# Performance work log

Measured on AMD Instinct MI355X. Metric: run time of the kernel, lower is better.

## Reference

```python
import jax, jax.numpy as jnp
import numpy as np

B, C, H, W = 8, 256, 48, 48
CK = 64  # C // k
WSCALE = 0.3 / np.sqrt(C)  # keep exp(QK^T) finite (original has no 1/sqrt(d) scaling)


def conv1x1(x, w, b):
    # x: (B,C,H,W), w: (O,C,1,1), b: (O,) -> (B,O,H,W)
    return jnp.einsum('bchw,oc->bohw', x, w[:, :, 0, 0]) + b[None, :, None, None]


def setup_inputs() -> dict:
    key = jax.random.key(0)
    ks = jax.random.split(key, 6)
    x = jax.random.normal(ks[0], (B, C, H, W), dtype=jnp.float32)
    qw = jax.random.normal(ks[1], (CK, C, 1, 1), dtype=jnp.float32) * WSCALE
    kw = jax.random.normal(ks[2], (CK, C, 1, 1), dtype=jnp.float32) * WSCALE
    vw = jax.random.normal(ks[3], (C, C, 1, 1), dtype=jnp.float32) * (1.0 / np.sqrt(C))
    gw = jax.random.normal(ks[4], (C, C, 1, 1), dtype=jnp.float32) * (1.0 / np.sqrt(C))
    zk = jnp.zeros((CK,), dtype=jnp.float32)
    zc = jnp.zeros((C,), dtype=jnp.float32)
    return {
        'x': x,
        'query_weight': qw, 'query_bias': zk,
        'key_weight': kw, 'key_bias': zk,
        'value_weight': vw, 'value_bias': zc,
        'gamma_weight': gw, 'gamma_bias': zc,
        'k': 4,
    }


def reference(x, query_weight, query_bias, key_weight, key_bias,
              value_weight, value_bias, gamma_weight, gamma_bias, k):
    b, c, h, w = x.shape
    n = h * w
    q = conv1x1(x, query_weight, query_bias).reshape(b, -1, n)   # (B,Ck,N)
    kk = conv1x1(x, key_weight, key_bias).reshape(b, -1, n)      # (B,Ck,N)
    # energy[b,i,j] = q_i . k_j  (queries on rows, no sqrt(d) scaling)
    energy = jnp.einsum('bci,bcj->bij', q, kk)                   # (B,N,N)
    energy = jnp.exp(energy)
    energy = energy / jnp.sum(energy, axis=2, keepdims=True)     # unnormalized-softmax over keys
    v = conv1x1(x, value_weight, value_bias).reshape(b, c, n)    # (B,C,N)
    # out[b,c,j] = sum_i v[b,c,i] * energy[b,i,j]  (faithful to torch.bmm(V, energy))
    out = jnp.einsum('bci,bij->bcj', v, energy).reshape(b, c, h, w)
    out = conv1x1(out, gamma_weight, gamma_bias)
    return out
```

## Files before the change

kernel.cpp:

```cpp
#include <hip/hip_runtime.h>

#define BATCH 8
#define CIN   256
#define NPIX  2304
#define CKD   64
#define NIT   (NPIX / 16)
#define NIC   (NPIX / 32)
#define NJB   (NPIX / 64)

typedef _Float16 f16;
typedef __attribute__((ext_vector_type(4))) _Float16 f16x4;
typedef __attribute__((ext_vector_type(8))) _Float16 f16x8;
typedef __attribute__((ext_vector_type(4))) float    f32x4;


__global__ __launch_bounds__(256) void cast_w(
    const float* __restrict__ qw, const float* __restrict__ kw,
    f16* __restrict__ Wqk)
{
    int idx = (blockIdx.x * 256 + threadIdx.x) * 4;
    const float* src = (idx < 16384) ? qw + idx : kw + (idx - 16384);
    float4 v = *(const float4*)src;
    f16x4 h = { (f16)v.x, (f16)v.y, (f16)v.z, (f16)v.w };
    *(f16x4*)&Wqk[idx] = h;
}

__global__ __launch_bounds__(256) void make_wgv(
    const float* __restrict__ gw, const float* __restrict__ vw,
    const float* __restrict__ vb,
    f16* __restrict__ Wgv, float* __restrict__ b2)
{
    const int o = blockIdx.x, c2 = threadIdx.x;
    float s = 0.f;
    for (int c = 0; c < CIN; ++c)
        s += gw[o * CIN + c] * vw[(size_t)c * CIN + c2];
    Wgv[(size_t)o * CIN + c2] = (f16)s;
    if (c2 == 0) {
        float sb = 0.f;
        for (int c = 0; c < CIN; ++c) sb += gw[o * CIN + c] * vb[c];
        b2[o] = sb;
    }
}

__global__ __launch_bounds__(256) void cast_xT(
    const float* __restrict__ x, f16* __restrict__ xT)
{
    __shared__ float s[64][65];
    const int t = threadIdx.x;
    const int n0 = blockIdx.x * 64, c0 = blockIdx.y * 64, b = blockIdx.z;
    const float* xb = x + ((size_t)b * CIN + c0) * NPIX + n0;

    const int cl = t >> 4, ng = (t & 15) * 4;
    #pragma unroll
    for (int p = 0; p < 4; ++p) {
        float4 v = *(const float4*)(xb + (size_t)(cl + 16 * p) * NPIX + ng);
        s[cl + 16 * p][ng + 0] = v.x;
        s[cl + 16 * p][ng + 1] = v.y;
        s[cl + 16 * p][ng + 2] = v.z;
        s[cl + 16 * p][ng + 3] = v.w;
    }
    __syncthreads();
    const int nl = t >> 2, cs = (t & 3) * 16;
    f16 h[16];
    #pragma unroll
    for (int j = 0; j < 16; ++j) h[j] = (f16)s[cs + j][nl];
    f16* gp = &xT[((size_t)b * NPIX + n0 + nl) * CIN + c0 + cs];
    *(f16x8*)gp       = *(f16x8*)&h[0];
    *(f16x8*)(gp + 8) = *(f16x8*)&h[8];
}

__global__ __launch_bounds__(256) void qk_conv_mfma(
    const f16* __restrict__ xT, const f16* __restrict__ Wqk,
    const float* __restrict__ qbias, const float* __restrict__ kbias,
    f16* __restrict__ q_blk, f16* __restrict__ k_blk)
{
    __shared__ __align__(16) f16 us[32 * 136];
    const int t = threadIdx.x, w = t >> 6, lane = t & 63;
    const int quad = lane >> 4, l16 = lane & 15;
    const int wm = w & 1, wn = w >> 1;
    const int n0 = blockIdx.x * 32, b = blockIdx.y;

    const f16* bp = xT + ((size_t)b * NPIX + n0 + 16 * wn + l16) * CIN;
    const f16* ap = Wqk + (size_t)(64 * wm + l16) * CIN;

    f32x4 acc[4];
    #pragma unroll
    for (int mt = 0; mt < 4; ++mt) acc[mt] = (f32x4){0.f, 0.f, 0.f, 0.f};

    #pragma unroll
    for (int kk = 0; kk < CIN; kk += 32) {
        f16x8 bf = *(const f16x8*)(bp + kk + quad * 8);
        #pragma unroll
        for (int mt = 0; mt < 4; ++mt) {
            f16x8 af = *(const f16x8*)(ap + (size_t)mt * 16 * CIN + kk + quad * 8);
            acc[mt] = __builtin_amdgcn_mfma_f32_16x16x32_f16(af, bf, acc[mt], 0, 0, 0);
        }
    }
    const float* bias = wm ? kbias - 64 : qbias;
    #pragma unroll
    for (int mt = 0; mt < 4; ++mt) {
        int ob = 64 * wm + 16 * mt + quad * 4;
        #pragma unroll
        for (int r = 0; r < 4; ++r)
            us[(16 * wn + l16) * 136 + ob + r] = (f16)(acc[mt][r] + bias[ob + r]);
    }
    __syncthreads();
    {
        int ks2 = t >> 7, nt = (t >> 6) & 1, ln = t & 63;
        const f16* usr = &us[(nt * 16 + (ln & 15)) * 136 + ks2 * 32 + (ln >> 4) * 8];
        size_t base = (((size_t)b * NIT + (n0 >> 4) + nt) * 2 + ks2) * 512 + ln * 8;
        *(f16x8*)&q_blk[base] = *(const f16x8*)(usr);
        *(f16x8*)&k_blk[base] = *(const f16x8*)(usr + 64);
    }
}

#define ESL 136
__global__ __launch_bounds__(256) void energy_S(
    const f16* __restrict__ q_blk, const f16* __restrict__ k_blk,
    float* __restrict__ Pred)
{
    __shared__ __align__(16) f16 es[64 * ESL];
    __shared__ float red2[2][128];
    const int t    = threadIdx.x;
    const int w    = t >> 6, lane = t & 63;
    const int quad = lane >> 4, l16 = lane & 15;
    const int j0 = blockIdx.x * 64, i0 = blockIdx.y * 128, b = blockIdx.z;
    const size_t ln8 = (size_t)lane * 8;
    const f16* qb = q_blk + (size_t)b * NIT * 2 * 512 + ln8;

    f32x4 acc[8];
    #pragma unroll
    for (int mt = 0; mt < 8; ++mt) acc[mt] = (f32x4){0.f, 0.f, 0.f, 0.f};

    #pragma unroll
    for (int ks = 0; ks < 2; ++ks) {
        f16x8 bf = *(const f16x8*)(k_blk +
            (((size_t)b * NIT + (j0 >> 4) + w) * 2 + ks) * 512 + ln8);
        #pragma unroll
        for (int mt = 0; mt < 8; ++mt) {
            f16x8 af = *(const f16x8*)(qb + ((size_t)((i0 >> 4) + mt) * 2 + ks) * 512);
            acc[mt] = __builtin_amdgcn_mfma_f32_16x16x32_f16(af, bf, acc[mt], 0, 0, 0);
        }
    }

    #pragma unroll
    for (int mt = 0; mt < 8; ++mt) {
        f16x4 h = { (f16)__expf(acc[mt][0]), (f16)__expf(acc[mt][1]),
                    (f16)__expf(acc[mt][2]), (f16)__expf(acc[mt][3]) };
        *(f16x4*)&es[(16 * w + l16) * ESL + 16 * mt + quad * 4] = h;
    }
    __syncthreads();
    {
        int i = t & 127, jq = t >> 7;
        float s = 0.f;
        #pragma unroll
        for (int jj = 0; jj < 32; ++jj)
            s += (float)es[(jq * 32 + jj) * ESL + i];
        red2[jq][i] = s;
    }
    __syncthreads();
    if (t < 128)
        Pred[((size_t)blockIdx.x * BATCH + b) * NPIX + i0 + t] =
            red2[0][t] + red2[1][t];
}

__global__ __launch_bounds__(256) void reduce_S(
    const float* __restrict__ Pred, float* __restrict__ S)
{
    const size_t BN = (size_t)BATCH * NPIX;
    size_t idx = (size_t)blockIdx.x * 256 + threadIdx.x;
    float s = 0.f;
    #pragma unroll
    for (int jb = 0; jb < NJB; ++jb)
        s += Pred[(size_t)jb * BN + idx];
    S[idx] = s;
}

__global__ __launch_bounds__(256) void v_conv_mfma(
    const f16* __restrict__ xT, const f16* __restrict__ Wv,
    const float* __restrict__ vbias, const float* __restrict__ S,
    f16* __restrict__ u_blk)
{
    __shared__ __align__(16) f16 smem[9216];
    f16* As = smem;
    f16* Bs = smem + 128 * 40;
    f16* us = smem;
    const int t = threadIdx.x, w = t >> 6, lane = t & 63;
    const int quad = lane >> 4, l16 = lane & 15;
    const int wm = w & 1, wn = w >> 1;
    const int i0 = blockIdx.x * 64, c0 = blockIdx.y * 128, b = blockIdx.z;
    const int sub = t >> 2, le = t & 3;
    const f16* srcA = Wv + (size_t)(c0 + sub) * CIN + le * 8;
    const f16* srcB = xT + ((size_t)b * NPIX + i0 + sub) * CIN + le * 8;
    const int ldsw = sub * 40 + le * 8;

    f32x4 acc[4][2];
    #pragma unroll
    for (int mt = 0; mt < 4; ++mt)
        #pragma unroll
        for (int nt = 0; nt < 2; ++nt)
            acc[mt][nt] = (f32x4){0.f, 0.f, 0.f, 0.f};

    for (int kk = 0; kk < CIN; kk += 32) {
        f16x8 ta0 = *(const f16x8*)(srcA + kk);
        f16x8 ta1 = *(const f16x8*)(srcA + (size_t)64 * CIN + kk);
        f16x8 tb0 = *(const f16x8*)(srcB + kk);
        __syncthreads();
        *(f16x8*)&As[ldsw]           = ta0;
        *(f16x8*)&As[64 * 40 + ldsw] = ta1;
        *(f16x8*)&Bs[ldsw]           = tb0;
        __syncthreads();
        f16x8 af[4], bf[2];
        #pragma unroll
        for (int mt = 0; mt < 4; ++mt)
            af[mt] = *(const f16x8*)&As[(64 * wm + 16 * mt + l16) * 40 + quad * 8];
        #pragma unroll
        for (int nt = 0; nt < 2; ++nt)
            bf[nt] = *(const f16x8*)&Bs[(32 * wn + 16 * nt + l16) * 40 + quad * 8];
        #pragma unroll
        for (int mt = 0; mt < 4; ++mt)
            #pragma unroll
            for (int nt = 0; nt < 2; ++nt)
                acc[mt][nt] = __builtin_amdgcn_mfma_f32_16x16x32_f16(
                    af[mt], bf[nt], acc[mt][nt], 0, 0, 0);
    }

    __syncthreads();
    #pragma unroll
    for (int nt = 0; nt < 2; ++nt) {
        int i = 32 * wn + 16 * nt + l16;
        float is = 1.0f / S[(size_t)b * NPIX + i0 + i];
        #pragma unroll
        for (int mt = 0; mt < 4; ++mt)
            #pragma unroll
            for (int r = 0; r < 4; ++r) {
                int c = 64 * wm + 16 * mt + quad * 4 + r;
                us[c * 72 + i] = (f16)((acc[mt][nt][r] + vbias[c0 + c]) * is);
            }
    }
    __syncthreads();
    #pragma unroll
    for (int p = 0; p < 4; ++p) {
        int g  = t + 256 * p;
        int ct = g >> 7, ic = (g >> 6) & 1, ln = g & 63;
        f16x8 v = *(const f16x8*)&us[(ct * 16 + (ln & 15)) * 72 + ic * 32 + (ln >> 4) * 8];
        *(f16x8*)&u_blk[(((size_t)b * 16 + (c0 >> 4) + ct) * NIC + (i0 >> 5) + ic) * 512 + ln * 8] = v;
    }
}

__global__ __launch_bounds__(1024, 4) void fused_bmm(
    const f16* __restrict__ q_blk, const f16* __restrict__ k_blk,
    const f16* __restrict__ u_blk, const float* __restrict__ gbias,
    float* __restrict__ out)
{
    extern __shared__ __align__(16) f16 es[];
    const int t = threadIdx.x, w = t >> 6, lane = t & 63;
    const int quad = lane >> 4, l16 = lane & 15;
    const int bid = blockIdx.x;
    const int b   = bid & 7;
    const int jb  = bid >> 3;
    const int j0  = jb * 64;
    const size_t ln8 = (size_t)lane * 8;

    const f16* qb = q_blk + (size_t)b * NIT * 2 * 512 + ln8;
    const f16* ub = u_blk + (size_t)b * 16 * NIC * 512 + ln8;

    const int jh = w & 3;
    const int iw = w >> 2;
    const int cg = w >> 1;
    const int jg = w & 1;
    const int CT0 = cg * 2;

    f16x8 kf[2];
    #pragma unroll
    for (int ks = 0; ks < 2; ++ks)
        kf[ks] = *(const f16x8*)(k_blk +
            (((size_t)b * NIT + (j0 >> 4) + jh) * 2 + ks) * 512 + ln8);

    const int woff = (quad >> 1) * 128 + l16 * 8 + (quad & 1) * 4;

    f32x4 acc[2][2];
    #pragma unroll
    for (int mt = 0; mt < 2; ++mt)
        #pragma unroll
        for (int jt = 0; jt < 2; ++jt)
            acc[mt][jt] = (f32x4){0.f, 0.f, 0.f, 0.f};

#define ULD(ct, icg) (*(const f16x8*)(ub + ((size_t)(CT0 + (ct)) * NIC + (icg)) * 512))

    #pragma unroll 1
    for (int gen = 0; gen < 9; ++gen) {
        const int t0 = gen * 16;
        #pragma unroll
        for (int s = 0; s < 4; ++s) {
            const int il = iw + 4 * s;
            const int gi = t0 + il;
            f16x8 q0 = *(const f16x8*)(qb + ((size_t)gi * 2 + 0) * 512);
            f16x8 q1 = *(const f16x8*)(qb + ((size_t)gi * 2 + 1) * 512);
            f32x4 e0 = (f32x4){0.f, 0.f, 0.f, 0.f};
            e0 = __builtin_amdgcn_mfma_f32_16x16x32_f16(q0, kf[0], e0, 0, 0, 0);
            e0 = __builtin_amdgcn_mfma_f32_16x16x32_f16(q1, kf[1], e0, 0, 0, 0);
            f16x4 h0 = { (f16)__expf(e0[0]), (f16)__expf(e0[1]),
                         (f16)__expf(e0[2]), (f16)__expf(e0[3]) };
            const int wo2 = ((il & 1) * 2) * 128 + woff;
            const int tb  = (il >> 1) * 4;
            *(f16x4*)&es[(size_t)(tb + jh) * 512 + wo2] = h0;
        }

        const int g0 = gen * 8;
        f16x8 ua0 = ULD(0, g0),     ua1 = ULD(1, g0);
        f16x8 na0 = ULD(0, g0 + 1), na1 = ULD(1, g0 + 1);
        asm volatile("s_waitcnt lgkmcnt(0)" ::: "memory");
        __builtin_amdgcn_s_barrier();

        __builtin_amdgcn_s_setprio(1);
        for (int ic2 = 0; ic2 < 8; ++ic2) {
            f16x8 fa0, fa1;
            if (ic2 + 2 < 8) { fa0 = ULD(0, g0 + ic2 + 2); fa1 = ULD(1, g0 + ic2 + 2); }
            f16x8 bf0 = *(const f16x8*)&es[(size_t)(ic2 * 4 + jg * 2 + 0) * 512 + ln8];
            f16x8 bf1 = *(const f16x8*)&es[(size_t)(ic2 * 4 + jg * 2 + 1) * 512 + ln8];
            acc[0][0] = __builtin_amdgcn_mfma_f32_16x16x32_f16(ua0, bf0, acc[0][0], 0, 0, 0);
            acc[1][0] = __builtin_amdgcn_mfma_f32_16x16x32_f16(ua1, bf0, acc[1][0], 0, 0, 0);
            acc[0][1] = __builtin_amdgcn_mfma_f32_16x16x32_f16(ua0, bf1, acc[0][1], 0, 0, 0);
            acc[1][1] = __builtin_amdgcn_mfma_f32_16x16x32_f16(ua1, bf1, acc[1][1], 0, 0, 0);
            ua0 = na0; ua1 = na1; na0 = fa0; na1 = fa1;
        }
        __builtin_amdgcn_s_setprio(0);
        __builtin_amdgcn_s_barrier();
    }
#undef ULD

    #pragma unroll
    for (int mt = 0; mt < 2; ++mt) {
        int cb = (CT0 + mt) * 16 + quad * 4;
        #pragma unroll
        for (int jt = 0; jt < 2; ++jt) {
            int j = j0 + (jg * 2 + jt) * 16 + l16;
            #pragma unroll
            for (int r = 0; r < 4; ++r)
                out[((size_t)b * CIN + cb + r) * NPIX + j] =
                    acc[mt][jt][r] + gbias[cb + r];
        }
    }
}

extern "C" void kernel_launch(void* const* d_in, const int* in_sizes, int n_in,
                              void* d_out, int out_size, void* d_ws, size_t ws_size,
                              hipStream_t stream) {
    const float* x   = (const float*)d_in[0];
    const float* qw  = (const float*)d_in[1];
    const float* qbv = (const float*)d_in[2];
    const float* kw  = (const float*)d_in[3];
    const float* kbv = (const float*)d_in[4];
    const float* vw  = (const float*)d_in[5];
    const float* vbv = (const float*)d_in[6];
    const float* gw  = (const float*)d_in[7];
    const float* gbv = (const float*)d_in[8];
    float* out = (float*)d_out;

    const size_t BCN  = (size_t)BATCH * CIN * NPIX;
    const size_t BN   = (size_t)BATCH * NPIX;
    const size_t BNCK = (size_t)BATCH * NPIX * CKD;

    f16* q_blk = (f16*)d_ws;
    f16* k_blk = q_blk + BNCK;
    f16* u_blk = k_blk + BNCK;
    f16* xT    = u_blk + BCN;
    f16* Wqk   = xT + BCN;
    f16* Wgv   = Wqk + 128 * 256;
    float* S   = (float*)(Wgv + 256 * 256);
    float* b2  = S + BN;
    float* Pred= b2 + 256;

    cast_w<<<32, 256, 0, stream>>>(qw, kw, Wqk);
    make_wgv<<<256, 256, 0, stream>>>(gw, vw, vbv, Wgv, b2);
    cast_xT<<<dim3(NPIX / 64, CIN / 64, BATCH), 256, 0, stream>>>(x, xT);
    qk_conv_mfma<<<dim3(NPIX / 32, BATCH), 256, 0, stream>>>(xT, Wqk, qbv, kbv, q_blk, k_blk);
    energy_S<<<dim3(NPIX / 64, NPIX / 128, BATCH), 256, 0, stream>>>(q_blk, k_blk, Pred);
    reduce_S<<<(int)(BN / 256), 256, 0, stream>>>(Pred, S);
    v_conv_mfma<<<dim3(NPIX / 64, CIN / 128, BATCH), 256, 0, stream>>>(xT, Wgv, b2, S, u_blk);
    fused_bmm<<<NJB * BATCH, 1024, 32 * 1024, stream>>>(q_blk, k_blk, u_blk, gbv, out);
}
```

Before: 226.6 us.

## Split fused_bmm channel range across two 512-thread blocks per j-tile

```diff
diff --git a/kernel.cpp b/kernel.cpp
--- a/kernel.cpp
+++ b/kernel.cpp
@@ -248,7 +248,7 @@
     }
 }
 
-__global__ __launch_bounds__(1024, 4) void fused_bmm(
+__global__ __launch_bounds__(512, 4) void fused_bmm(
     const f16* __restrict__ q_blk, const f16* __restrict__ k_blk,
     const f16* __restrict__ u_blk, const float* __restrict__ gbias,
     float* __restrict__ out)
@@ -258,18 +258,18 @@
     const int quad = lane >> 4, l16 = lane & 15;
     const int bid = blockIdx.x;
     const int b   = bid & 7;
-    const int jb  = bid >> 3;
+    const int r   = bid >> 3;
+    const int ch  = r & 1;
+    const int jb  = r >> 1;
     const int j0  = jb * 64;
     const size_t ln8 = (size_t)lane * 8;
 
     const f16* qb = q_blk + (size_t)b * NIT * 2 * 512 + ln8;
     const f16* ub = u_blk + (size_t)b * 16 * NIC * 512 + ln8;
 
-    const int jh = w & 3;
-    const int iw = w >> 2;
-    const int cg = w >> 1;
-    const int jg = w & 1;
-    const int CT0 = cg * 2;
+    const int jh    = w & 3;
+    const int ihalf = w >> 2;
+    const int CT = ch * 8 + w;
 
     f16x8 kf[2];
     #pragma unroll
@@ -279,21 +279,19 @@
 
     const int woff = (quad >> 1) * 128 + l16 * 8 + (quad & 1) * 4;
 
-    f32x4 acc[2][2];
-    #pragma unroll
-    for (int mt = 0; mt < 2; ++mt)
-        #pragma unroll
-        for (int jt = 0; jt < 2; ++jt)
-            acc[mt][jt] = (f32x4){0.f, 0.f, 0.f, 0.f};
-
-#define ULD(ct, icg) (*(const f16x8*)(ub + ((size_t)(CT0 + (ct)) * NIC + (icg)) * 512))
+    f32x4 acc[4];
+    #pragma unroll
+    for (int jt = 0; jt < 4; ++jt)
+        acc[jt] = (f32x4){0.f, 0.f, 0.f, 0.f};
+
+#define ULD(icg) (*(const f16x8*)(ub + ((size_t)CT * NIC + (icg)) * 512))
 
     #pragma unroll 1
     for (int gen = 0; gen < 9; ++gen) {
         const int t0 = gen * 16;
         #pragma unroll
-        for (int s = 0; s < 4; ++s) {
-            const int il = iw + 4 * s;
+        for (int s = 0; s < 8; ++s) {
+            const int il = ihalf + 2 * s;
             const int gi = t0 + il;
             f16x8 q0 = *(const f16x8*)(qb + ((size_t)gi * 2 + 0) * 512);
             f16x8 q1 = *(const f16x8*)(qb + ((size_t)gi * 2 + 1) * 512);
@@ -308,38 +306,36 @@
         }
 
         const int g0 = gen * 8;
-        f16x8 ua0 = ULD(0, g0),     ua1 = ULD(1, g0);
-        f16x8 na0 = ULD(0, g0 + 1), na1 = ULD(1, g0 + 1);
+        f16x8 ua = ULD(g0);
+        f16x8 na = ULD(g0 + 1);
         asm volatile("s_waitcnt lgkmcnt(0)" ::: "memory");
         __builtin_amdgcn_s_barrier();
 
         __builtin_amdgcn_s_setprio(1);
         for (int ic2 = 0; ic2 < 8; ++ic2) {
-            f16x8 fa0, fa1;
-            if (ic2 + 2 < 8) { fa0 = ULD(0, g0 + ic2 + 2); fa1 = ULD(1, g0 + ic2 + 2); }
-            f16x8 bf0 = *(const f16x8*)&es[(size_t)(ic2 * 4 + jg * 2 + 0) * 512 + ln8];
-            f16x8 bf1 = *(const f16x8*)&es[(size_t)(ic2 * 4 + jg * 2 + 1) * 512 + ln8];
-            acc[0][0] = __builtin_amdgcn_mfma_f32_16x16x32_f16(ua0, bf0, acc[0][0], 0, 0, 0);
-            acc[1][0] = __builtin_amdgcn_mfma_f32_16x16x32_f16(ua1, bf0, acc[1][0], 0, 0, 0);
-            acc[0][1] = __builtin_amdgcn_mfma_f32_16x16x32_f16(ua0, bf1, acc[0][1], 0, 0, 0);
-            acc[1][1] = __builtin_amdgcn_mfma_f32_16x16x32_f16(ua1, bf1, acc[1][1], 0, 0, 0);
-            ua0 = na0; ua1 = na1; na0 = fa0; na1 = fa1;
+            f16x8 fa;
+            if (ic2 + 2 < 8) fa = ULD(g0 + ic2 + 2);
+            #pragma unroll
+            for (int jt = 0; jt < 4; ++jt) {
+                f16x8 bf = *(const f16x8*)&es[(size_t)(ic2 * 4 + jt) * 512 + ln8];
+                acc[jt] = __builtin_amdgcn_mfma_f32_16x16x32_f16(ua, bf, acc[jt], 0, 0, 0);
+            }
+            ua = na; na = fa;
         }
         __builtin_amdgcn_s_setprio(0);
         __builtin_amdgcn_s_barrier();
     }
 #undef ULD
 
-    #pragma unroll
-    for (int mt = 0; mt < 2; ++mt) {
-        int cb = (CT0 + mt) * 16 + quad * 4;
-        #pragma unroll
-        for (int jt = 0; jt < 2; ++jt) {
-            int j = j0 + (jg * 2 + jt) * 16 + l16;
+    {
+        const int cb = CT * 16 + quad * 4;
+        #pragma unroll
+        for (int jt = 0; jt < 4; ++jt) {
+            int j = j0 + jt * 16 + l16;
             #pragma unroll
-            for (int r = 0; r < 4; ++r)
-                out[((size_t)b * CIN + cb + r) * NPIX + j] =
-                    acc[mt][jt][r] + gbias[cb + r];
+            for (int r2 = 0; r2 < 4; ++r2)
+                out[((size_t)b * CIN + cb + r2) * NPIX + j] =
+                    acc[jt][r2] + gbias[cb + r2];
         }
     }
 }
@@ -379,5 +375,5 @@
     energy_S<<<dim3(NPIX / 64, NPIX / 128, BATCH), 256, 0, stream>>>(q_blk, k_blk, Pred);
     reduce_S<<<(int)(BN / 256), 256, 0, stream>>>(Pred, S);
     v_conv_mfma<<<dim3(NPIX / 64, CIN / 128, BATCH), 256, 0, stream>>>(xT, Wgv, b2, S, u_blk);
-    fused_bmm<<<NJB * BATCH, 1024, 32 * 1024, stream>>>(q_blk, k_blk, u_blk, gbv, out);
-}
+    fused_bmm<<<NJB * 2 * BATCH, 512, 32 * 1024, stream>>>(q_blk, k_blk, u_blk, gbv, out);
+}
```

Measured after the change: 210.9 us. 6.9% less time.

## Double-buffer exp tiles in fused_bmm with 512 threads, fold S reduction and weight prep

Applied to the files above, without the earlier changes.

```diff
diff --git a/kernel.cpp b/kernel.cpp
--- a/kernel.cpp
+++ b/kernel.cpp
@@ -14,31 +14,30 @@
 typedef __attribute__((ext_vector_type(4))) float    f32x4;
 
 
-__global__ __launch_bounds__(256) void cast_w(
+__global__ __launch_bounds__(256) void prep_w(
     const float* __restrict__ qw, const float* __restrict__ kw,
-    f16* __restrict__ Wqk)
-{
-    int idx = (blockIdx.x * 256 + threadIdx.x) * 4;
-    const float* src = (idx < 16384) ? qw + idx : kw + (idx - 16384);
-    float4 v = *(const float4*)src;
-    f16x4 h = { (f16)v.x, (f16)v.y, (f16)v.z, (f16)v.w };
-    *(f16x4*)&Wqk[idx] = h;
-}
-
-__global__ __launch_bounds__(256) void make_wgv(
     const float* __restrict__ gw, const float* __restrict__ vw,
     const float* __restrict__ vb,
-    f16* __restrict__ Wgv, float* __restrict__ b2)
-{
-    const int o = blockIdx.x, c2 = threadIdx.x;
-    float s = 0.f;
-    for (int c = 0; c < CIN; ++c)
-        s += gw[o * CIN + c] * vw[(size_t)c * CIN + c2];
-    Wgv[(size_t)o * CIN + c2] = (f16)s;
-    if (c2 == 0) {
-        float sb = 0.f;
-        for (int c = 0; c < CIN; ++c) sb += gw[o * CIN + c] * vb[c];
-        b2[o] = sb;
+    f16* __restrict__ Wqk, f16* __restrict__ Wgv, float* __restrict__ b2)
+{
+    const int bid = blockIdx.x, t = threadIdx.x;
+    if (bid < 32) {
+        int idx = (bid * 256 + t) * 4;
+        const float* src = (idx < 16384) ? qw + idx : kw + (idx - 16384);
+        float4 v = *(const float4*)src;
+        f16x4 h = { (f16)v.x, (f16)v.y, (f16)v.z, (f16)v.w };
+        *(f16x4*)&Wqk[idx] = h;
+    } else {
+        const int o = bid - 32, c2 = t;
+        float s = 0.f;
+        for (int c = 0; c < CIN; ++c)
+            s += gw[o * CIN + c] * vw[(size_t)c * CIN + c2];
+        Wgv[(size_t)o * CIN + c2] = (f16)s;
+        if (c2 == 0) {
+            float sb = 0.f;
+            for (int c = 0; c < CIN; ++c) sb += gw[o * CIN + c] * vb[c];
+            b2[o] = sb;
+        }
     }
 }
 
@@ -164,24 +163,13 @@
             red2[0][t] + red2[1][t];
 }
 
-__global__ __launch_bounds__(256) void reduce_S(
-    const float* __restrict__ Pred, float* __restrict__ S)
-{
-    const size_t BN = (size_t)BATCH * NPIX;
-    size_t idx = (size_t)blockIdx.x * 256 + threadIdx.x;
-    float s = 0.f;
-    #pragma unroll
-    for (int jb = 0; jb < NJB; ++jb)
-        s += Pred[(size_t)jb * BN + idx];
-    S[idx] = s;
-}
-
 __global__ __launch_bounds__(256) void v_conv_mfma(
     const f16* __restrict__ xT, const f16* __restrict__ Wv,
-    const float* __restrict__ vbias, const float* __restrict__ S,
+    const float* __restrict__ vbias, const float* __restrict__ Pred,
     f16* __restrict__ u_blk)
 {
     __shared__ __align__(16) f16 smem[9216];
+    __shared__ float Sinv[64];
     f16* As = smem;
     f16* Bs = smem + 128 * 40;
     f16* us = smem;
@@ -194,6 +182,15 @@
     const f16* srcB = xT + ((size_t)b * NPIX + i0 + sub) * CIN + le * 8;
     const int ldsw = sub * 40 + le * 8;
 
+    if (t < 64) {
+        const float* pp = Pred + (size_t)b * NPIX + i0 + t;
+        float s = 0.f;
+        #pragma unroll
+        for (int jb2 = 0; jb2 < NJB; ++jb2)
+            s += pp[(size_t)jb2 * BATCH * NPIX];
+        Sinv[t] = 1.0f / s;
+    }
+
     f32x4 acc[4][2];
     #pragma unroll
     for (int mt = 0; mt < 4; ++mt)
@@ -229,7 +226,7 @@
     #pragma unroll
     for (int nt = 0; nt < 2; ++nt) {
         int i = 32 * wn + 16 * nt + l16;
-        float is = 1.0f / S[(size_t)b * NPIX + i0 + i];
+        float is = Sinv[i];
         #pragma unroll
         for (int mt = 0; mt < 4; ++mt)
             #pragma unroll
@@ -248,7 +245,7 @@
     }
 }
 
-__global__ __launch_bounds__(1024, 4) void fused_bmm(
+__global__ __launch_bounds__(512, 2) void fused_bmm(
     const f16* __restrict__ q_blk, const f16* __restrict__ k_blk,
     const f16* __restrict__ u_blk, const float* __restrict__ gbias,
     float* __restrict__ out)
@@ -267,9 +264,7 @@
 
     const int jh = w & 3;
     const int iw = w >> 2;
-    const int cg = w >> 1;
-    const int jg = w & 1;
-    const int CT0 = cg * 2;
+    const int CT0 = w * 2;
 
     f16x8 kf[2];
     #pragma unroll
@@ -279,63 +274,75 @@
 
     const int woff = (quad >> 1) * 128 + l16 * 8 + (quad & 1) * 4;
 
-    f32x4 acc[2][2];
+    f32x4 acc[2][4];
     #pragma unroll
     for (int mt = 0; mt < 2; ++mt)
         #pragma unroll
-        for (int jt = 0; jt < 2; ++jt)
+        for (int jt = 0; jt < 4; ++jt)
             acc[mt][jt] = (f32x4){0.f, 0.f, 0.f, 0.f};
 
 #define ULD(ct, icg) (*(const f16x8*)(ub + ((size_t)(CT0 + (ct)) * NIC + (icg)) * 512))
 
+#define PHASE1(g, bsel) do {                                                   \
+    const int t0_ = (g) * 16;                                                  \
+    _Pragma("unroll 4")                                                        \
+    for (int s_ = 0; s_ < 8; ++s_) {                                           \
+        const int il_ = iw + 2 * s_;                                           \
+        const int gi_ = t0_ + il_;                                             \
+        f16x8 q0_ = *(const f16x8*)(qb + ((size_t)gi_ * 2 + 0) * 512);         \
+        f16x8 q1_ = *(const f16x8*)(qb + ((size_t)gi_ * 2 + 1) * 512);         \
+        f32x4 e0_ = (f32x4){0.f, 0.f, 0.f, 0.f};                               \
+        e0_ = __builtin_amdgcn_mfma_f32_16x16x32_f16(q0_, kf[0], e0_, 0, 0, 0);\
+        e0_ = __builtin_amdgcn_mfma_f32_16x16x32_f16(q1_, kf[1], e0_, 0, 0, 0);\
+        f16x4 h0_ = { (f16)__expf(e0_[0]), (f16)__expf(e0_[1]),                \
+                      (f16)__expf(e0_[2]), (f16)__expf(e0_[3]) };              \
+        const int wo2_ = ((il_ & 1) * 2) * 128 + woff;                         \
+        const int tb_  = (il_ >> 1) * 4;                                       \
+        *(f16x4*)&es[(size_t)((bsel) * 32 + tb_ + jh) * 512 + wo2_] = h0_;     \
+    }                                                                          \
+} while (0)
+
+#define BAR() do {                                                             \
+    asm volatile("s_waitcnt lgkmcnt(0)" ::: "memory");                         \
+    __builtin_amdgcn_s_barrier();                                              \
+} while (0)
+
+    f16x8 ua0 = ULD(0, 0), ua1 = ULD(1, 0);
+    f16x8 na0 = ULD(0, 1), na1 = ULD(1, 1);
+    PHASE1(0, 0);
+    BAR();
+
     #pragma unroll 1
-    for (int gen = 0; gen < 9; ++gen) {
-        const int t0 = gen * 16;
-        #pragma unroll
-        for (int s = 0; s < 4; ++s) {
-            const int il = iw + 4 * s;
-            const int gi = t0 + il;
-            f16x8 q0 = *(const f16x8*)(qb + ((size_t)gi * 2 + 0) * 512);
-            f16x8 q1 = *(const f16x8*)(qb + ((size_t)gi * 2 + 1) * 512);
-            f32x4 e0 = (f32x4){0.f, 0.f, 0.f, 0.f};
-            e0 = __builtin_amdgcn_mfma_f32_16x16x32_f16(q0, kf[0], e0, 0, 0, 0);
-            e0 = __builtin_amdgcn_mfma_f32_16x16x32_f16(q1, kf[1], e0, 0, 0, 0);
-            f16x4 h0 = { (f16)__expf(e0[0]), (f16)__expf(e0[1]),
-                         (f16)__expf(e0[2]), (f16)__expf(e0[3]) };
-            const int wo2 = ((il & 1) * 2) * 128 + woff;
-            const int tb  = (il >> 1) * 4;
-            *(f16x4*)&es[(size_t)(tb + jh) * 512 + wo2] = h0;
-        }
-
-        const int g0 = gen * 8;
-        f16x8 ua0 = ULD(0, g0),     ua1 = ULD(1, g0);
-        f16x8 na0 = ULD(0, g0 + 1), na1 = ULD(1, g0 + 1);
-        asm volatile("s_waitcnt lgkmcnt(0)" ::: "memory");
-        __builtin_amdgcn_s_barrier();
-
+    for (int g = 0; g < 9; ++g) {
+        if (g + 1 < 9) PHASE1(g + 1, (g + 1) & 1);
         __builtin_amdgcn_s_setprio(1);
+        #pragma unroll
         for (int ic2 = 0; ic2 < 8; ++ic2) {
+            const int k = g * 8 + ic2;
             f16x8 fa0, fa1;
-            if (ic2 + 2 < 8) { fa0 = ULD(0, g0 + ic2 + 2); fa1 = ULD(1, g0 + ic2 + 2); }
-            f16x8 bf0 = *(const f16x8*)&es[(size_t)(ic2 * 4 + jg * 2 + 0) * 512 + ln8];
-            f16x8 bf1 = *(const f16x8*)&es[(size_t)(ic2 * 4 + jg * 2 + 1) * 512 + ln8];
-            acc[0][0] = __builtin_amdgcn_mfma_f32_16x16x32_f16(ua0, bf0, acc[0][0], 0, 0, 0);
-            acc[1][0] = __builtin_amdgcn_mfma_f32_16x16x32_f16(ua1, bf0, acc[1][0], 0, 0, 0);
-            acc[0][1] = __builtin_amdgcn_mfma_f32_16x16x32_f16(ua0, bf1, acc[0][1], 0, 0, 0);
-            acc[1][1] = __builtin_amdgcn_mfma_f32_16x16x32_f16(ua1, bf1, acc[1][1], 0, 0, 0);
+            if (k + 2 < NIC) { fa0 = ULD(0, k + 2); fa1 = ULD(1, k + 2); }
+            #pragma unroll
+            for (int jt = 0; jt < 4; ++jt) {
+                f16x8 bf = *(const f16x8*)&es[
+                    (size_t)((g & 1) * 32 + ic2 * 4 + jt) * 512 + ln8];
+                acc[0][jt] = __builtin_amdgcn_mfma_f32_16x16x32_f16(ua0, bf, acc[0][jt], 0, 0, 0);
+                acc[1][jt] = __builtin_amdgcn_mfma_f32_16x16x32_f16(ua1, bf, acc[1][jt], 0, 0, 0);
+            }
             ua0 = na0; ua1 = na1; na0 = fa0; na1 = fa1;
         }
         __builtin_amdgcn_s_setprio(0);
-        __builtin_amdgcn_s_barrier();
+        BAR();
     }
 #undef ULD
+#undef PHASE1
+#undef BAR
 
     #pragma unroll
     for (int mt = 0; mt < 2; ++mt) {
-        int cb = (CT0 + mt) * 16 + quad * 4;
-        #pragma unroll
-        for (int jt = 0; jt < 2; ++jt) {
-            int j = j0 + (jg * 2 + jt) * 16 + l16;
+        int cb = 32 * w + 16 * mt + quad * 4;
+        #pragma unroll
+        for (int jt = 0; jt < 4; ++jt) {
+            int j = j0 + 16 * jt + l16;
             #pragma unroll
             for (int r = 0; r < 4; ++r)
                 out[((size_t)b * CIN + cb + r) * NPIX + j] =
@@ -368,16 +375,13 @@
     f16* xT    = u_blk + BCN;
     f16* Wqk   = xT + BCN;
     f16* Wgv   = Wqk + 128 * 256;
-    float* S   = (float*)(Wgv + 256 * 256);
-    float* b2  = S + BN;
+    float* b2  = (float*)(Wgv + 256 * 256);
     float* Pred= b2 + 256;
 
-    cast_w<<<32, 256, 0, stream>>>(qw, kw, Wqk);
-    make_wgv<<<256, 256, 0, stream>>>(gw, vw, vbv, Wgv, b2);
+    prep_w<<<288, 256, 0, stream>>>(qw, kw, gw, vw, vbv, Wqk, Wgv, b2);
     cast_xT<<<dim3(NPIX / 64, CIN / 64, BATCH), 256, 0, stream>>>(x, xT);
     qk_conv_mfma<<<dim3(NPIX / 32, BATCH), 256, 0, stream>>>(xT, Wqk, qbv, kbv, q_blk, k_blk);
     energy_S<<<dim3(NPIX / 64, NPIX / 128, BATCH), 256, 0, stream>>>(q_blk, k_blk, Pred);
-    reduce_S<<<(int)(BN / 256), 256, 0, stream>>>(Pred, S);
-    v_conv_mfma<<<dim3(NPIX / 64, CIN / 128, BATCH), 256, 0, stream>>>(xT, Wgv, b2, S, u_blk);
-    fused_bmm<<<NJB * BATCH, 1024, 32 * 1024, stream>>>(q_blk, k_blk, u_blk, gbv, out);
-}
+    v_conv_mfma<<<dim3(NPIX / 64, CIN / 128, BATCH), 256, 0, stream>>>(xT, Wgv, b2, Pred, u_blk);
+    fused_bmm<<<NJB * BATCH, 512, 64 * 1024, stream>>>(q_blk, k_blk, u_blk, gbv, out);
+}
```

After: 200.2 us. -11.7%, faster.
